# Performance work log

Measured on AMD Instinct MI355X. Metric: run time of the kernel, lower is better.

The kernel has to match this reference:

```python
import jax, jax.numpy as jnp
import numpy as np

# Quantization constants (from init_kwargs)
INPUT_SCALE = 0.05
OUTPUT_SCALE = 0.1
OUTPUT_ZERO_POINT = 0
FEATURE_BITWIDTH = 8
Q_MIN = -(1 << (FEATURE_BITWIDTH - 1))       # -128
Q_MAX = (1 << (FEATURE_BITWIDTH - 1)) - 1    #  127

B, IN_F, OUT_F = 8192, 4096, 4096


def setup_inputs() -> dict:
    key = jax.random.key(0)
    k_x, k_w, k_b, k_s = jax.random.split(key, 4)
    # int8 quantized activations and weights
    x = jax.random.randint(k_x, (B, IN_F), Q_MIN, Q_MAX + 1, dtype=jnp.int8)
    weight = jax.random.randint(k_w, (OUT_F, IN_F), Q_MIN, Q_MAX + 1, dtype=jnp.int8)
    # shifted quantized bias (int32)
    bias = jax.random.randint(k_b, (OUT_F,), -1000, 1000, dtype=jnp.int32)
    # per-output-channel weight scale (positive floats)
    weight_scale = jax.random.uniform(k_s, (OUT_F,), dtype=jnp.float32, minval=0.001, maxval=0.01)
    return {"x": x, "weight": weight, "bias": bias, "weight_scale": weight_scale}


def reference(x, weight, bias, weight_scale):
    # int32-accumulated GEMM: [B, in] @ [in, out] + bias -> [B, out]
    acc = jnp.matmul(x.astype(jnp.int32), weight.astype(jnp.int32).T,
                     preferred_element_type=jnp.int32) + bias[None, :]
    # dequant/requant epilogue with per-channel scale
    out = acc.astype(jnp.float32) * (INPUT_SCALE * weight_scale[None, :] / OUTPUT_SCALE) + OUTPUT_ZERO_POINT
    out = jnp.clip(jnp.round(out), Q_MIN, Q_MAX).astype(jnp.int8)
    return out
```

## Files before the change

kernel.cpp:

```cpp
#include <hip/hip_runtime.h>
#include <cstdint>
#include <cstddef>

#define M_DIM 8192
#define N_DIM 4096
#define K_DIM 4096

#define BM 256
#define BN 256

using i32x4 = __attribute__((ext_vector_type(4))) int;

__device__ __forceinline__ void async_load16(const void* g, void* l) {
    __builtin_amdgcn_global_load_lds(
        (const __attribute__((address_space(1))) void*)g,
        (__attribute__((address_space(3))) void*)l,
        16, 0, 0);
}

__global__ __launch_bounds__(256) void pack_i8_kernel(const int4* __restrict__ xsrc,
                                                      int* __restrict__ xdst,
                                                      const int4* __restrict__ wsrc,
                                                      int* __restrict__ wdst,
                                                      int nxblocks) {
    const bool isw = (int)blockIdx.x >= nxblocks;
    const int4* src = isw ? wsrc : xsrc;
    int*       dst  = isw ? wdst : xdst;
    const long bb   = isw ? ((long)blockIdx.x - nxblocks) : (long)blockIdx.x;
    const long base = bb * 1024 + threadIdx.x;
#pragma unroll
    for (int j = 0; j < 4; ++j) {
        const long i = base + 256 * j;
        const int4 v = src[i];
        dst[i] = (v.x & 0xff) | ((v.y & 0xff) << 8) | ((v.z & 0xff) << 16) | (v.w << 24);
    }
}

__global__ __launch_bounds__(512, 2) void qgemm_i8_kernel(const int8_t* __restrict__ A,
                                                          const int8_t* __restrict__ B,
                                                          const int* __restrict__ bias,
                                                          const float* __restrict__ wscale,
                                                          int* __restrict__ C) {
    __shared__ int8_t LDS[131072];

    const int tid  = threadIdx.x;
    const int wave = tid >> 6;
    const int lane = tid & 63;
    const int wm = wave >> 2;
    const int wn = wave & 3;
    const int bm = blockIdx.y;
    const int bn = blockIdx.x;

    const int8_t* Ab = A + (size_t)bm * BM * K_DIM;
    const int8_t* Bb = B + (size_t)bn * BN * K_DIM;

    const int l8 = lane >> 3;
    const int l7 = lane & 7;
    const int8_t* Ag = Ab + (size_t)(wave * 16 + l8) * K_DIM + ((l7 ^ l8) * 16);
    const int8_t* Bg = Bb + (size_t)(wave * 16 + l8) * K_DIM + ((l7 ^ l8) * 16);
    const int sdst = wave * 2048;

    const int l15 = lane & 15;
    const int qh  = lane >> 4;
    const int a_off0 = wm * 8192 + l15 * 128 + ((qh ^ l7) * 16);
    const int a_off1 = a_off0 ^ 64;
    const int b_off0 = 65536 + wn * 4096 + l15 * 128 + ((qh ^ l7) * 16);
    const int b_off1 = b_off0 ^ 64;

    i32x4 acc[4][4][2] = {};
    i32x4 af[4][2];
    i32x4 bf[2][2][2];

#define ISSUE_HT(GB, REG, BUF, HH, T) do { \
    async_load16((GB) + (size_t)((HH) * 128)     * K_DIM + (size_t)(T) * 128, \
                 &LDS[(REG) + (BUF) * 32768 + (HH) * 16384 + sdst]); \
    async_load16((GB) + (size_t)((HH) * 128 + 8) * K_DIM + (size_t)(T) * 128, \
                 &LDS[(REG) + (BUF) * 32768 + (HH) * 16384 + sdst + 1024]); \
} while (0)

#define LOAD_AF(BUF, MH) do { \
    _Pragma("unroll") \
    for (int mi = 0; mi < 4; ++mi) { \
        af[mi][0] = *(const i32x4*)&LDS[a_off0 + (BUF) * 32768 + (MH) * 16384 + mi * 2048]; \
        af[mi][1] = *(const i32x4*)&LDS[a_off1 + (BUF) * 32768 + (MH) * 16384 + mi * 2048]; \
    } \
} while (0)

#define LOAD_BF(BUF, NH) do { \
    _Pragma("unroll") \
    for (int ni = 0; ni < 2; ++ni) { \
        bf[NH][ni][0] = *(const i32x4*)&LDS[b_off0 + (BUF) * 32768 + (NH) * 16384 + ni * 2048]; \
        bf[NH][ni][1] = *(const i32x4*)&LDS[b_off1 + (BUF) * 32768 + (NH) * 16384 + ni * 2048]; \
    } \
} while (0)

#define VM6 asm volatile("s_waitcnt vmcnt(6)" ::: "memory")
#define VM0 asm volatile("s_waitcnt vmcnt(0)" ::: "memory")

#define PHASE(LOADS, QD, NHB, ISSUES, CHK) do { \
    LOADS; \
    ISSUES; \
    CHK; \
    __builtin_amdgcn_s_barrier(); \
    __builtin_amdgcn_s_setprio(1); \
    _Pragma("unroll") \
    for (int mi = 0; mi < 4; ++mi) { \
        _Pragma("unroll") \
        for (int ni = 0; ni < 2; ++ni) { \
            acc[QD][mi][ni] = __builtin_amdgcn_mfma_i32_16x16x64_i8(af[mi][0], bf[NHB][ni][0], acc[QD][mi][ni], 0, 0, 0); \
            acc[QD][mi][ni] = __builtin_amdgcn_mfma_i32_16x16x64_i8(af[mi][1], bf[NHB][ni][1], acc[QD][mi][ni], 0, 0, 0); \
        } \
    } \
    __builtin_amdgcn_s_setprio(0); \
    __builtin_amdgcn_s_barrier(); \
} while (0)

    ISSUE_HT(Ag, 0,     0, 0, 0);
    ISSUE_HT(Bg, 65536, 0, 0, 0);
    ISSUE_HT(Bg, 65536, 0, 1, 0);
    ISSUE_HT(Ag, 0,     0, 1, 0);
    ISSUE_HT(Ag, 0,     1, 0, 1);
    ISSUE_HT(Bg, 65536, 1, 1, 1);
    ISSUE_HT(Ag, 0,     1, 1, 1);
    asm volatile("s_waitcnt vmcnt(10)" ::: "memory");
    __builtin_amdgcn_s_barrier();

    for (int i = 0; i < 16; ++i) {
        const int V = 2 * i + 1;
        const int W = 2 * i + 2;
        const int X = 2 * i + 3;
        const bool more = (i < 15);

        PHASE({ LOAD_AF(0, 0); LOAD_BF(0, 0); }, 0, 0,
              { ISSUE_HT(Bg, 65536, 1, 0, V); }, VM6);
        PHASE({ LOAD_BF(0, 1); }, 1, 1,
              { if (more) ISSUE_HT(Ag, 0,     0, 0, W); }, VM6);
        PHASE({ LOAD_AF(0, 1); }, 2, 1,
              { if (more) ISSUE_HT(Bg, 65536, 0, 1, W); }, VM6);
        PHASE({}, 3, 0,
              { if (more) ISSUE_HT(Ag, 0,     0, 1, W); },
              { if (more) { VM6; } else { VM0; } });
        PHASE({ LOAD_AF(1, 0); LOAD_BF(1, 0); }, 0, 0,
              { if (more) ISSUE_HT(Bg, 65536, 0, 0, W); }, VM6);
        PHASE({ LOAD_BF(1, 1); }, 1, 1,
              { if (more) ISSUE_HT(Ag, 0,     1, 0, X); }, VM6);
        PHASE({ LOAD_AF(1, 1); }, 2, 1,
              { if (more) ISSUE_HT(Bg, 65536, 1, 1, X); }, VM6);
        PHASE({}, 3, 0,
              { if (more) ISSUE_HT(Ag, 0,     1, 1, X); }, VM6);
    }

#undef PHASE
#undef VM0
#undef VM6
#undef LOAD_BF
#undef LOAD_AF
#undef ISSUE_HT

    const int col16 = lane & 15;
    const int rquad = (lane >> 4) * 4;
#pragma unroll
    for (int qd = 0; qd < 4; ++qd) {
        const int mh = qd >> 1;
        const int nh = (qd >> 1) ^ (qd & 1);
#pragma unroll
        for (int ni = 0; ni < 2; ++ni) {
            const int col = bn * BN + nh * 128 + wn * 32 + ni * 16 + col16;
            float s = 0.05f * wscale[col];
            s = s / 0.1f;
            const float bz = (float)bias[col];
#pragma unroll
            for (int mi = 0; mi < 4; ++mi) {
                const int row0 = bm * BM + mh * 128 + wm * 64 + mi * 16 + rquad;
#pragma unroll
                for (int r = 0; r < 4; ++r) {
                    float v = ((float)acc[qd][mi][ni][r] + bz) * s;
                    v = rintf(v);
                    v = fminf(fmaxf(v, -128.0f), 127.0f);
                    C[(size_t)(row0 + r) * N_DIM + col] = (int)v;
                }
            }
        }
    }
}

extern "C" void kernel_launch(void* const* d_in, const int* in_sizes, int n_in,
                              void* d_out, int out_size, void* d_ws, size_t ws_size,
                              hipStream_t stream) {
    const int*   x32    = (const int*)d_in[0];
    const int*   w32    = (const int*)d_in[1];
    const int*   bias   = (const int*)d_in[2];
    const float* wscale = (const float*)d_in[3];
    int*         out    = (int*)d_out;

    int8_t* xp = (int8_t*)d_ws;
    int8_t* wp = xp + (size_t)M_DIM * K_DIM;

    {
        const int nxblocks = (int)((long)M_DIM * K_DIM / 4 / 1024);
        const int nwblocks = (int)((long)N_DIM * K_DIM / 4 / 1024);
        pack_i8_kernel<<<nxblocks + nwblocks, 256, 0, stream>>>(
            (const int4*)x32, (int*)xp, (const int4*)w32, (int*)wp, nxblocks);
    }

    dim3 grid(N_DIM / BN, M_DIM / BM);
    qgemm_i8_kernel<<<grid, 512, 0, stream>>>(xp, wp, bias, wscale, out);
}
```

Before: 389.2 us.

## Merge pipeline phases to halve barriers per K-step with double quadrant MFMA

Restructures the main loop from eight phases per iteration to four. Each phase now computes two accumulator quadrants and issues two half-tile async loads, with the vmcnt thresholds and prologue prefetch order adjusted to match. This halves the number of barrier pairs and waitcnt points per K tile, cutting synchronisation overhead. The cost is longer gaps between refills and less slack for global loads, which can expose memory latency.

```diff
diff --git a/kernel.cpp b/kernel.cpp
--- a/kernel.cpp
+++ b/kernel.cpp
@@ -94,10 +94,11 @@
     } \
 } while (0)
 
-#define VM6 asm volatile("s_waitcnt vmcnt(6)" ::: "memory")
+#define VM8 asm volatile("s_waitcnt vmcnt(8)" ::: "memory")
+#define VM4 asm volatile("s_waitcnt vmcnt(4)" ::: "memory")
 #define VM0 asm volatile("s_waitcnt vmcnt(0)" ::: "memory")
 
-#define PHASE(LOADS, QD, NHB, ISSUES, CHK) do { \
+#define PHASE2(LOADS, QDA, NA, QDB, NB, ISSUES, CHK) do { \
     LOADS; \
     ISSUES; \
     CHK; \
@@ -107,8 +108,16 @@
     for (int mi = 0; mi < 4; ++mi) { \
         _Pragma("unroll") \
         for (int ni = 0; ni < 2; ++ni) { \
-            acc[QD][mi][ni] = __builtin_amdgcn_mfma_i32_16x16x64_i8(af[mi][0], bf[NHB][ni][0], acc[QD][mi][ni], 0, 0, 0); \
-            acc[QD][mi][ni] = __builtin_amdgcn_mfma_i32_16x16x64_i8(af[mi][1], bf[NHB][ni][1], acc[QD][mi][ni], 0, 0, 0); \
+            acc[QDA][mi][ni] = __builtin_amdgcn_mfma_i32_16x16x64_i8(af[mi][0], bf[NA][ni][0], acc[QDA][mi][ni], 0, 0, 0); \
+            acc[QDA][mi][ni] = __builtin_amdgcn_mfma_i32_16x16x64_i8(af[mi][1], bf[NA][ni][1], acc[QDA][mi][ni], 0, 0, 0); \
+        } \
+    } \
+    _Pragma("unroll") \
+    for (int mi = 0; mi < 4; ++mi) { \
+        _Pragma("unroll") \
+        for (int ni = 0; ni < 2; ++ni) { \
+            acc[QDB][mi][ni] = __builtin_amdgcn_mfma_i32_16x16x64_i8(af[mi][0], bf[NB][ni][0], acc[QDB][mi][ni], 0, 0, 0); \
+            acc[QDB][mi][ni] = __builtin_amdgcn_mfma_i32_16x16x64_i8(af[mi][1], bf[NB][ni][1], acc[QDB][mi][ni], 0, 0, 0); \
         } \
     } \
     __builtin_amdgcn_s_setprio(0); \
@@ -120,9 +129,8 @@
     ISSUE_HT(Bg, 65536, 0, 1, 0);
     ISSUE_HT(Ag, 0,     0, 1, 0);
     ISSUE_HT(Ag, 0,     1, 0, 1);
-    ISSUE_HT(Bg, 65536, 1, 1, 1);
-    ISSUE_HT(Ag, 0,     1, 1, 1);
-    asm volatile("s_waitcnt vmcnt(10)" ::: "memory");
+    ISSUE_HT(Bg, 65536, 1, 0, 1);
+    asm volatile("s_waitcnt vmcnt(6)" ::: "memory");
     __builtin_amdgcn_s_barrier();
 
     for (int i = 0; i < 16; ++i) {
@@ -131,28 +139,24 @@
         const int X = 2 * i + 3;
         const bool more = (i < 15);
 
-        PHASE({ LOAD_AF(0, 0); LOAD_BF(0, 0); }, 0, 0,
-              { ISSUE_HT(Bg, 65536, 1, 0, V); }, VM6);
-        PHASE({ LOAD_BF(0, 1); }, 1, 1,
-              { if (more) ISSUE_HT(Ag, 0,     0, 0, W); }, VM6);
-        PHASE({ LOAD_AF(0, 1); }, 2, 1,
-              { if (more) ISSUE_HT(Bg, 65536, 0, 1, W); }, VM6);
-        PHASE({}, 3, 0,
-              { if (more) ISSUE_HT(Ag, 0,     0, 1, W); },
-              { if (more) { VM6; } else { VM0; } });
-        PHASE({ LOAD_AF(1, 0); LOAD_BF(1, 0); }, 0, 0,
-              { if (more) ISSUE_HT(Bg, 65536, 0, 0, W); }, VM6);
-        PHASE({ LOAD_BF(1, 1); }, 1, 1,
-              { if (more) ISSUE_HT(Ag, 0,     1, 0, X); }, VM6);
-        PHASE({ LOAD_AF(1, 1); }, 2, 1,
-              { if (more) ISSUE_HT(Bg, 65536, 1, 1, X); }, VM6);
-        PHASE({}, 3, 0,
-              { if (more) ISSUE_HT(Ag, 0,     1, 1, X); }, VM6);
-    }
-
-#undef PHASE
+        PHASE2({ LOAD_AF(0, 0); LOAD_BF(0, 0); LOAD_BF(0, 1); }, 0, 0, 1, 1,
+               { ISSUE_HT(Bg, 65536, 1, 1, V); ISSUE_HT(Ag, 0, 1, 1, V); },
+               VM8);
+        PHASE2({ LOAD_AF(0, 1); }, 2, 1, 3, 0,
+               { if (more) { ISSUE_HT(Ag, 0, 0, 0, W); ISSUE_HT(Bg, 65536, 0, 0, W); } },
+               { if (more) { VM4; } else { VM0; } });
+        PHASE2({ LOAD_AF(1, 0); LOAD_BF(1, 0); LOAD_BF(1, 1); }, 0, 0, 1, 1,
+               { if (more) { ISSUE_HT(Bg, 65536, 0, 1, W); ISSUE_HT(Ag, 0, 0, 1, W); } },
+               { if (more) { VM8; } else { VM0; } });
+        PHASE2({ LOAD_AF(1, 1); }, 2, 1, 3, 0,
+               { if (more) { ISSUE_HT(Ag, 0, 1, 0, X); ISSUE_HT(Bg, 65536, 1, 0, X); } },
+               { if (more) { VM4; } else { VM0; } });
+    }
+
+#undef PHASE2
 #undef VM0
-#undef VM6
+#undef VM4
+#undef VM8
 #undef LOAD_BF
 #undef LOAD_AF
 #undef ISSUE_HT
```

Result: no change. 395.1 us (+1.5%).
